# Kernel tuning notes

Measured on AMD Instinct MI355X. Metric: run time of the kernel, lower is better.

## Reference

```python
import jax, jax.numpy as jnp
import numpy as np
import math

B, T, C, H = 4, 2048, 1024, 16
D = C // H  # head dim


def setup_inputs() -> dict:
    key = jax.random.key(0)
    ks = jax.random.split(key, 8)
    s = 1.0 / math.sqrt(C)
    return {
        "q": jax.random.normal(ks[0], (B, T, C), jnp.float32),
        "k": jax.random.normal(ks[1], (B, T, C), jnp.float32),
        "v": jax.random.normal(ks[2], (B, T, C), jnp.float32),
        "Wq": jax.random.normal(ks[3], (C, C), jnp.float32) * s,
        "bq": jnp.zeros((C,), jnp.float32),
        "Wk": jax.random.normal(ks[4], (C, C), jnp.float32) * s,
        "bk": jnp.zeros((C,), jnp.float32),
        "Wv": jax.random.normal(ks[5], (C, C), jnp.float32) * s,
        "bv": jnp.zeros((C,), jnp.float32),
        "Wo": jax.random.normal(ks[6], (C, C), jnp.float32) * s,
        "bo": jnp.zeros((C,), jnp.float32),
    }


def reference(q, k, v, Wq, bq, Wk, bk, Wv, bv, Wo, bo):
    # Linear projections (torch Linear: x @ W.T + b; here W stored as [in,out])
    qh = (q @ Wq + bq).reshape(B, T, H, D).transpose(0, 2, 1, 3)  # [B,H,T,D]
    kh = (k @ Wk + bk).reshape(B, T, H, D).transpose(0, 2, 1, 3)
    vh = (v @ Wv + bv).reshape(B, T, H, D).transpose(0, 2, 1, 3)
    scores = jnp.einsum("bhqd,bhkd->bhqk", qh, kh) * (1.0 / math.sqrt(D))
    att = jax.nn.softmax(scores, axis=-1)
    y = jnp.einsum("bhqk,bhkd->bhqd", att, vh)  # [B,H,T,D]
    y = y.transpose(0, 2, 1, 3).reshape(B, T, C)
    return y @ Wo + bo
```

## Files before the change

kernel.cpp:

```cpp
#include <hip/hip_runtime.h>
#include <hip/hip_bf16.h>


#define B_ 4
#define T_ 2048
#define C_ 1024
#define H_ 16
#define D_ 64
#define M_ (B_*T_)

typedef __attribute__((ext_vector_type(4))) float f32x4;
typedef __attribute__((ext_vector_type(8))) short short8;

__device__ __forceinline__ unsigned short f2bf(float f) {
  unsigned u = __float_as_uint(f);
  u = (u + 0x7fffu + ((u >> 16) & 1u)) >> 16;
  return (unsigned short)u;
}

__device__ __forceinline__ unsigned cvtpk_bf16(float lo, float hi) {
  unsigned r;
  asm("v_cvt_pk_bf16_f32 %0, %1, %2" : "=v"(r) : "v"(lo), "v"(hi));
  return r;
}

__device__ __forceinline__ void gload_lds16(const void* g, void* l) {
  __builtin_amdgcn_global_load_lds(
      (__attribute__((address_space(1))) void*)(g),
      (__attribute__((address_space(3))) void*)(l), 16, 0, 0);
}

__global__ __launch_bounds__(256) void prep_all(const float* __restrict__ q,
                                                const float* __restrict__ k,
                                                const float* __restrict__ v,
                                                const float* __restrict__ W0,
                                                const float* __restrict__ W1,
                                                const float* __restrict__ W2,
                                                const float* __restrict__ W3,
                                                unsigned short* __restrict__ qb,
                                                unsigned short* __restrict__ kb,
                                                unsigned short* __restrict__ vb,
                                                unsigned short* __restrict__ T0,
                                                unsigned short* __restrict__ T1,
                                                unsigned short* __restrict__ T2,
                                                unsigned short* __restrict__ T3) {
  __shared__ float tile[64][65];
  const int id = blockIdx.x;
  if (id < 24576) {
    const int arr = id >> 13;
    const int blk = id & 8191;
    const float* s = (arr == 0) ? q : (arr == 1) ? k : v;
    unsigned short* d = (arr == 0) ? qb : (arr == 1) ? kb : vb;
    int i = blk * 256 + threadIdx.x;
    float4 x = ((const float4*)s)[i];
    ushort4 o = { f2bf(x.x), f2bf(x.y), f2bf(x.z), f2bf(x.w) };
    ((ushort4*)d)[i] = o;
  } else {
    const int tid = id - 24576;
    const int z = tid >> 8;
    const int tl = tid & 255;
    const float* W = (z == 0) ? W0 : (z == 1) ? W1 : (z == 2) ? W2 : W3;
    unsigned short* WT = (z == 0) ? T0 : (z == 1) ? T1 : (z == 2) ? T2 : T3;
    const int tr = (tl >> 4) * 64;
    const int tc = (tl & 15) * 64;
    const int t = threadIdx.x;
    const int cg = (t & 15) * 4;
    const int rw = t >> 4;
#pragma unroll
    for (int it = 0; it < 4; ++it) {
      int r = it * 16 + rw;
      float4 x = *(const float4*)(W + (size_t)(tr + r) * C_ + tc + cg);
      tile[r][cg] = x.x; tile[r][cg + 1] = x.y; tile[r][cg + 2] = x.z; tile[r][cg + 3] = x.w;
    }
    __syncthreads();
#pragma unroll
    for (int it = 0; it < 4; ++it) {
      int n = it * 16 + rw;
      ushort4 o = { f2bf(tile[cg][n]), f2bf(tile[cg + 1][n]),
                    f2bf(tile[cg + 2][n]), f2bf(tile[cg + 3][n]) };
      *(ushort4*)(WT + (size_t)(tc + n) * C_ + tr + cg) = o;
    }
  }
}

__device__ __forceinline__ void gemm_core(const unsigned short* __restrict__ A,
                                          const unsigned short* __restrict__ BT,
                                          int bm, int bn, int wid, int lane,
                                          unsigned short* As, unsigned short* Bs,
                                          f32x4 acc[4][4]) {
  const int wr = wid >> 1, wc = wid & 1;
  const int lr = lane & 15, lk = lane >> 4;
  for (int k0 = 0; k0 < C_; k0 += 64) {
    __syncthreads();
#pragma unroll
    for (int it = 0; it < 4; ++it) {
      int wo = it * 256 + wid * 64;
      int o = wo + lane;
      gload_lds16(A + (size_t)(bm * 128 + (o >> 3)) * C_ + k0 + (o & 7) * 8, As + wo * 8);
    }
#pragma unroll
    for (int it = 0; it < 4; ++it) {
      int wo = it * 256 + wid * 64;
      int o = wo + lane;
      gload_lds16(BT + (size_t)(bn * 128 + (o >> 3)) * C_ + k0 + (o & 7) * 8, Bs + wo * 8);
    }
    __syncthreads();

    short8 af[2][4], bf[2][4];
#pragma unroll
    for (int kc = 0; kc < 2; ++kc) {
#pragma unroll
      for (int mi = 0; mi < 4; ++mi)
        af[kc][mi] = *(const short8*)(As + (wr * 64 + mi * 16 + lr) * 64 + kc * 32 + lk * 8);
#pragma unroll
      for (int ni = 0; ni < 4; ++ni)
        bf[kc][ni] = *(const short8*)(Bs + (wc * 64 + ni * 16 + lr) * 64 + kc * 32 + lk * 8);
    }
#pragma unroll
    for (int kc = 0; kc < 2; ++kc)
#pragma unroll
      for (int mi = 0; mi < 4; ++mi)
#pragma unroll
        for (int ni = 0; ni < 4; ++ni)
          acc[mi][ni] = __builtin_amdgcn_mfma_f32_16x16x32_bf16(af[kc][mi], bf[kc][ni],
                                                                acc[mi][ni], 0, 0, 0);
  }
}

__global__ __launch_bounds__(256) void gemm_qkv(const unsigned short* __restrict__ qb,
                                                const unsigned short* __restrict__ kb,
                                                const unsigned short* __restrict__ vb,
                                                const unsigned short* __restrict__ wqt,
                                                const unsigned short* __restrict__ wkt,
                                                const unsigned short* __restrict__ wvt,
                                                const float* __restrict__ bq,
                                                const float* __restrict__ bk,
                                                const float* __restrict__ bv,
                                                unsigned short* __restrict__ Qh,
                                                unsigned short* __restrict__ Kh,
                                                unsigned short* __restrict__ VTh) {
  __shared__ unsigned short As[128 * 64];
  __shared__ unsigned short Bs[128 * 64];
  const int y = blockIdx.y;
  const unsigned short* A  = (y == 0) ? qb  : (y == 1) ? kb  : vb;
  const unsigned short* BT = (y == 0) ? wqt : (y == 1) ? wkt : wvt;
  const float* bias        = (y == 0) ? bq  : (y == 1) ? bk  : bv;
  unsigned short* O        = (y == 0) ? Qh  : (y == 1) ? Kh  : VTh;
  const bool vt = (y == 2);
  const int id = blockIdx.x;
  const int wk = (id & 7) * 64 + (id >> 3);
  const int bn = wk & 7;
  const int bm = wk >> 3;
  const int wid = threadIdx.x >> 6, lane = threadIdx.x & 63;
  const int wr = wid >> 1, wc = wid & 1;
  const int lr = lane & 15, lk = lane >> 4;
  f32x4 acc[4][4] = {};
  gemm_core(A, BT, bm, bn, wid, lane, As, Bs, acc);

  float bvv[4];
#pragma unroll
  for (int ni = 0; ni < 4; ++ni) bvv[ni] = bias[bn * 128 + wc * 64 + ni * 16 + lr];
#pragma unroll
  for (int mi = 0; mi < 4; ++mi)
#pragma unroll
    for (int ni = 0; ni < 4; ++ni) {
      int n = bn * 128 + wc * 64 + ni * 16 + lr;
      int h = n >> 6, d = n & 63;
#pragma unroll
      for (int j = 0; j < 4; ++j) {
        int m = bm * 128 + wr * 64 + mi * 16 + lk * 4 + j;
        int b = m >> 11, tt = m & (T_ - 1);
        size_t idx = vt ? ((size_t)(b * H_ + h) * D_ + d) * T_ + tt
                        : ((size_t)(b * H_ + h) * T_ + tt) * D_ + d;
        O[idx] = f2bf(acc[mi][ni][j] + bvv[ni]);
      }
    }
}

__global__ __launch_bounds__(256) void gemm_out(const unsigned short* __restrict__ A,
                                                const unsigned short* __restrict__ BT,
                                                const float* __restrict__ bias,
                                                float* __restrict__ O) {
  __shared__ unsigned short As[128 * 64];
  __shared__ unsigned short Bs[128 * 64];
  const int id = blockIdx.x;
  const int wk = (id & 7) * 64 + (id >> 3);
  const int bn = wk & 7;
  const int bm = wk >> 3;
  const int wid = threadIdx.x >> 6, lane = threadIdx.x & 63;
  const int wr = wid >> 1, wc = wid & 1;
  const int lr = lane & 15, lk = lane >> 4;
  f32x4 acc[4][4] = {};
  gemm_core(A, BT, bm, bn, wid, lane, As, Bs, acc);

  float bvv[4];
#pragma unroll
  for (int ni = 0; ni < 4; ++ni) bvv[ni] = bias[bn * 128 + wc * 64 + ni * 16 + lr];
#pragma unroll
  for (int mi = 0; mi < 4; ++mi)
#pragma unroll
    for (int ni = 0; ni < 4; ++ni) {
      int n = bn * 128 + wc * 64 + ni * 16 + lr;
#pragma unroll
      for (int j = 0; j < 4; ++j) {
        int m = bm * 128 + wr * 64 + mi * 16 + lk * 4 + j;
        O[(size_t)m * C_ + n] = acc[mi][ni][j] + bvv[ni];
      }
    }
}

__global__ __launch_bounds__(256) void attn_fwd(const unsigned short* __restrict__ Qg,
                                                const unsigned short* __restrict__ Kg,
                                                const unsigned short* __restrict__ Vg,
                                                unsigned short* __restrict__ Y) {
  __shared__ unsigned short Ks[2][64 * 64];
  __shared__ unsigned short Vs[2][64 * 64];
  __shared__ unsigned short Ps[64 * 64];
  const int id = blockIdx.x;
  const int wk = (id & 7) * 256 + (id >> 3);
  const int bh = wk >> 5;
  const int qt = wk & 31;
  const int b = bh >> 4, h = bh & 15;
  const int t = threadIdx.x;
  const int wid = t >> 6, lane = t & 63;
  const int lr = lane & 15, lk = lane >> 4;
  const size_t hoff = (size_t)bh * T_ * D_;
  const unsigned short* Qh = Qg + hoff + (size_t)qt * 64 * D_;
  const unsigned short* Kh = Kg + hoff;
  const unsigned short* Vh = Vg + hoff;
  const int NT = T_ / 64;

  auto stage = [&](int bfi, int kt) {
    const unsigned short* Ksrc = Kh + (size_t)kt * 64 * D_;
#pragma unroll
    for (int it = 0; it < 2; ++it) {
      int wo = it * 256 + wid * 64;
      int o = wo + lane;
      int r = o >> 3, c = (o & 7) ^ (r & 7);
      gload_lds16(Ksrc + (size_t)r * D_ + c * 8, Ks[bfi] + wo * 8);
      gload_lds16(Vh + (size_t)r * T_ + kt * 64 + c * 8, Vs[bfi] + wo * 8);
    }
  };

#pragma unroll
  for (int it = 0; it < 2; ++it) {
    int wo = it * 256 + wid * 64;
    int o = wo + lane;
    int r = o >> 3, c = (o & 7) ^ (r & 7);
    gload_lds16(Qh + (size_t)r * D_ + c * 8, Ps + wo * 8);
  }
  stage(0, 0);
  __syncthreads();
  short8 qf[2];
#pragma unroll
  for (int kc = 0; kc < 2; ++kc)
    qf[kc] = *(const short8*)(Ps + (wid * 16 + lr) * 64 + (((kc * 4 + lk) ^ (lr & 7)) * 8));
  asm volatile("s_waitcnt lgkmcnt(0)" ::: "memory");

  f32x4 yacc[4] = {};
  float mrow = -1e30f, lsum = 0.f;
  const float SCL = 0.125f;
  const float L2E = 1.44269504088896f;
  const float C1 = SCL * L2E;

  int cur = 0;
  for (int kt = 0; kt < NT; ++kt) {
    if (kt + 1 < NT) stage(cur ^ 1, kt + 1);

    f32x4 sacc[4] = {};
    __builtin_amdgcn_s_setprio(1);
#pragma unroll
    for (int kc = 0; kc < 2; ++kc)
#pragma unroll
      for (int nt = 0; nt < 4; ++nt) {
        short8 kf = *(const short8*)(Ks[cur] + (nt * 16 + lr) * 64 +
                                     (((kc * 4 + lk) ^ (lr & 7)) * 8));
        sacc[nt] = __builtin_amdgcn_mfma_f32_16x16x32_bf16(kf, qf[kc], sacc[nt], 0, 0, 0);
      }
    __builtin_amdgcn_s_setprio(0);

    float m0 = fmaxf(fmaxf(sacc[0][0], sacc[0][1]), fmaxf(sacc[0][2], sacc[0][3]));
#pragma unroll
    for (int nt = 1; nt < 4; ++nt)
      m0 = fmaxf(m0, fmaxf(fmaxf(sacc[nt][0], sacc[nt][1]),
                           fmaxf(sacc[nt][2], sacc[nt][3])));
    m0 = fmaxf(m0, __shfl_xor(m0, 16, 64));
    m0 = fmaxf(m0, __shfl_xor(m0, 32, 64));
    float mx = m0 * SCL;
    if (__any(mx - mrow > 8.0f)) {
      float mn = fmaxf(mrow, mx);
      float esc = exp2f((mrow - mn) * L2E);
      mrow = mn;
      lsum *= esc;
      float e0 = __shfl(esc, 4 * lk + 0, 16);
      float e1 = __shfl(esc, 4 * lk + 1, 16);
      float e2 = __shfl(esc, 4 * lk + 2, 16);
      float e3 = __shfl(esc, 4 * lk + 3, 16);
#pragma unroll
      for (int nt = 0; nt < 4; ++nt) {
        yacc[nt][0] *= e0; yacc[nt][1] *= e1;
        yacc[nt][2] *= e2; yacc[nt][3] *= e3;
      }
    }
    float ml2 = mrow * L2E;
    float rs = 0.f;
#pragma unroll
    for (int nt = 0; nt < 4; ++nt) {
      float p0 = exp2f(sacc[nt][0] * C1 - ml2);
      float p1 = exp2f(sacc[nt][1] * C1 - ml2);
      float p2 = exp2f(sacc[nt][2] * C1 - ml2);
      float p3 = exp2f(sacc[nt][3] * C1 - ml2);
      rs += (p0 + p1) + (p2 + p3);
      uint2 pv;
      pv.x = cvtpk_bf16(p0, p1);
      pv.y = cvtpk_bf16(p2, p3);
      *(uint2*)(Ps + (wid * 16 + lr) * 64 +
                (((2 * nt + (lk >> 1)) ^ (lr & 7)) * 8 + (lk & 1) * 4)) = pv;
    }
    rs += __shfl_xor(rs, 16, 64);
    rs += __shfl_xor(rs, 32, 64);
    lsum += rs;
    asm volatile("s_waitcnt lgkmcnt(0)" ::: "memory");

    __builtin_amdgcn_s_setprio(1);
#pragma unroll
    for (int kc = 0; kc < 2; ++kc) {
      short8 pa = *(const short8*)(Ps + (wid * 16 + lr) * 64 +
                                   (((kc * 4 + lk) ^ (lr & 7)) * 8));
#pragma unroll
      for (int nt = 0; nt < 4; ++nt) {
        short8 vf = *(const short8*)(Vs[cur] + (nt * 16 + lr) * 64 +
                                     (((kc * 4 + lk) ^ (lr & 7)) * 8));
        yacc[nt] = __builtin_amdgcn_mfma_f32_16x16x32_bf16(pa, vf, yacc[nt], 0, 0, 0);
      }
    }
    __builtin_amdgcn_s_setprio(0);

    __syncthreads();
    cur ^= 1;
  }

  float rinv = __builtin_amdgcn_rcpf(lsum);
  float r0 = __shfl(rinv, 4 * lk + 0, 16);
  float r1 = __shfl(rinv, 4 * lk + 1, 16);
  float r2 = __shfl(rinv, 4 * lk + 2, 16);
  float r3 = __shfl(rinv, 4 * lk + 3, 16);
#pragma unroll
  for (int nt = 0; nt < 4; ++nt) {
    int row = qt * 64 + wid * 16 + lk * 4;
    int col = h * D_ + nt * 16 + lr;
    size_t base = ((size_t)b * T_ + row) * C_ + col;
    Y[base]          = f2bf(yacc[nt][0] * r0);
    Y[base + C_]     = f2bf(yacc[nt][1] * r1);
    Y[base + 2 * C_] = f2bf(yacc[nt][2] * r2);
    Y[base + 3 * C_] = f2bf(yacc[nt][3] * r3);
  }
}

extern "C" void kernel_launch(void* const* d_in, const int* in_sizes, int n_in,
                              void* d_out, int out_size, void* d_ws, size_t ws_size,
                              hipStream_t stream) {
  const float* q  = (const float*)d_in[0];
  const float* k  = (const float*)d_in[1];
  const float* v  = (const float*)d_in[2];
  const float* Wq = (const float*)d_in[3];
  const float* bq = (const float*)d_in[4];
  const float* Wk = (const float*)d_in[5];
  const float* bk = (const float*)d_in[6];
  const float* Wv = (const float*)d_in[7];
  const float* bv = (const float*)d_in[8];
  const float* Wo = (const float*)d_in[9];
  const float* bo = (const float*)d_in[10];

  char* ws = (char*)d_ws;
  const size_t S1 = (size_t)M_ * C_ * 2;
  const size_t SW = (size_t)C_ * C_ * 2;
  unsigned short* qb  = (unsigned short*)(ws);
  unsigned short* kb  = (unsigned short*)(ws + S1);
  unsigned short* vb  = (unsigned short*)(ws + 2 * S1);
  unsigned short* wqt = (unsigned short*)(ws + 3 * S1);
  unsigned short* wkt = (unsigned short*)(ws + 3 * S1 + SW);
  unsigned short* wvt = (unsigned short*)(ws + 3 * S1 + 2 * SW);
  unsigned short* wot = (unsigned short*)(ws + 3 * S1 + 3 * SW);
  unsigned short* Qh  = (unsigned short*)(ws + 3 * S1 + 4 * SW);
  unsigned short* Kh  = (unsigned short*)(ws + 4 * S1 + 4 * SW);
  unsigned short* VTh = (unsigned short*)(ws + 5 * S1 + 4 * SW);
  unsigned short* Yw  = (unsigned short*)(ws + 6 * S1 + 4 * SW);

  prep_all<<<25600, 256, 0, stream>>>(q, k, v, Wq, Wk, Wv, Wo,
                                      qb, kb, vb, wqt, wkt, wvt, wot);

  const int ngemm = (C_ / 128) * (M_ / 128);
  gemm_qkv<<<dim3(ngemm, 3), 256, 0, stream>>>(qb, kb, vb, wqt, wkt, wvt,
                                               bq, bk, bv, Qh, Kh, VTh);

  attn_fwd<<<(T_ / 64) * B_ * H_, 256, 0, stream>>>(Qh, Kh, VTh, Yw);

  gemm_out<<<ngemm, 256, 0, stream>>>(Yw, wot, bo, (float*)d_out);
}
```

Before: 432.7 us.

## Split each key tile across two wave groups in attention with final merge

The attention block grows from 4 to 8 waves. Each pair of waves handles the same 16 query rows, but each wave processes a different 32-key half of every 64-key tile. Each wave keeps its own running max, sum and output accumulator, and the two partial results are combined through LDS in an online-softmax merge at the end. This roughly doubles the waves available to hide latency and halves the MFMA and softmax work per wave, at the cost of an extra LDS merge, a final barrier, and higher per-block thread and register demand.

```diff
diff --git a/kernel.cpp b/kernel.cpp
--- a/kernel.cpp
+++ b/kernel.cpp
@@ -209,7 +209,7 @@
     }
 }
 
-__global__ __launch_bounds__(256) void attn_fwd(const unsigned short* __restrict__ Qg,
+__global__ __launch_bounds__(512) void attn_fwd(const unsigned short* __restrict__ Qg,
                                                 const unsigned short* __restrict__ Kg,
                                                 const unsigned short* __restrict__ Vg,
                                                 unsigned short* __restrict__ Y) {
@@ -223,6 +223,7 @@
   const int b = bh >> 4, h = bh & 15;
   const int t = threadIdx.x;
   const int wid = t >> 6, lane = t & 63;
+  const int wq = wid & 3, kh = wid >> 2;
   const int lr = lane & 15, lk = lane >> 4;
   const size_t hoff = (size_t)bh * T_ * D_;
   const unsigned short* Qh = Qg + hoff + (size_t)qt * 64 * D_;
@@ -230,32 +231,23 @@
   const unsigned short* Vh = Vg + hoff;
   const int NT = T_ / 64;
 
+  const int o = wid * 64 + lane;
+  const int sr = o >> 3, sc = (o & 7) ^ ((o >> 3) & 7);
+  const int sbase = wid * 512;
+
   auto stage = [&](int bfi, int kt) {
-    const unsigned short* Ksrc = Kh + (size_t)kt * 64 * D_;
-#pragma unroll
-    for (int it = 0; it < 2; ++it) {
-      int wo = it * 256 + wid * 64;
-      int o = wo + lane;
-      int r = o >> 3, c = (o & 7) ^ (r & 7);
-      gload_lds16(Ksrc + (size_t)r * D_ + c * 8, Ks[bfi] + wo * 8);
-      gload_lds16(Vh + (size_t)r * T_ + kt * 64 + c * 8, Vs[bfi] + wo * 8);
-    }
+    gload_lds16(Kh + (size_t)kt * 64 * D_ + (size_t)sr * D_ + sc * 8, Ks[bfi] + sbase);
+    gload_lds16(Vh + (size_t)sr * T_ + kt * 64 + sc * 8, Vs[bfi] + sbase);
   };
 
-#pragma unroll
-  for (int it = 0; it < 2; ++it) {
-    int wo = it * 256 + wid * 64;
-    int o = wo + lane;
-    int r = o >> 3, c = (o & 7) ^ (r & 7);
-    gload_lds16(Qh + (size_t)r * D_ + c * 8, Ps + wo * 8);
-  }
+  gload_lds16(Qh + (size_t)sr * D_ + sc * 8, Ps + sbase);
   stage(0, 0);
   __syncthreads();
   short8 qf[2];
 #pragma unroll
   for (int kc = 0; kc < 2; ++kc)
-    qf[kc] = *(const short8*)(Ps + (wid * 16 + lr) * 64 + (((kc * 4 + lk) ^ (lr & 7)) * 8));
-  asm volatile("s_waitcnt lgkmcnt(0)" ::: "memory");
+    qf[kc] = *(const short8*)(Ps + (wq * 16 + lr) * 64 + (((kc * 4 + lk) ^ (lr & 7)) * 8));
+  __syncthreads();
 
   f32x4 yacc[4] = {};
   float mrow = -1e30f, lsum = 0.f;
@@ -267,23 +259,20 @@
   for (int kt = 0; kt < NT; ++kt) {
     if (kt + 1 < NT) stage(cur ^ 1, kt + 1);
 
-    f32x4 sacc[4] = {};
+    f32x4 sacc[2] = {};
     __builtin_amdgcn_s_setprio(1);
 #pragma unroll
     for (int kc = 0; kc < 2; ++kc)
 #pragma unroll
-      for (int nt = 0; nt < 4; ++nt) {
-        short8 kf = *(const short8*)(Ks[cur] + (nt * 16 + lr) * 64 +
+      for (int ntl = 0; ntl < 2; ++ntl) {
+        short8 kf = *(const short8*)(Ks[cur] + (kh * 32 + ntl * 16 + lr) * 64 +
                                      (((kc * 4 + lk) ^ (lr & 7)) * 8));
-        sacc[nt] = __builtin_amdgcn_mfma_f32_16x16x32_bf16(kf, qf[kc], sacc[nt], 0, 0, 0);
+        sacc[ntl] = __builtin_amdgcn_mfma_f32_16x16x32_bf16(kf, qf[kc], sacc[ntl], 0, 0, 0);
       }
     __builtin_amdgcn_s_setprio(0);
 
     float m0 = fmaxf(fmaxf(sacc[0][0], sacc[0][1]), fmaxf(sacc[0][2], sacc[0][3]));
-#pragma unroll
-    for (int nt = 1; nt < 4; ++nt)
-      m0 = fmaxf(m0, fmaxf(fmaxf(sacc[nt][0], sacc[nt][1]),
-                           fmaxf(sacc[nt][2], sacc[nt][3])));
+    m0 = fmaxf(m0, fmaxf(fmaxf(sacc[1][0], sacc[1][1]), fmaxf(sacc[1][2], sacc[1][3])));
     m0 = fmaxf(m0, __shfl_xor(m0, 16, 64));
     m0 = fmaxf(m0, __shfl_xor(m0, 32, 64));
     float mx = m0 * SCL;
@@ -305,17 +294,17 @@
     float ml2 = mrow * L2E;
     float rs = 0.f;
 #pragma unroll
-    for (int nt = 0; nt < 4; ++nt) {
-      float p0 = exp2f(sacc[nt][0] * C1 - ml2);
-      float p1 = exp2f(sacc[nt][1] * C1 - ml2);
-      float p2 = exp2f(sacc[nt][2] * C1 - ml2);
-      float p3 = exp2f(sacc[nt][3] * C1 - ml2);
+    for (int ntl = 0; ntl < 2; ++ntl) {
+      float p0 = exp2f(sacc[ntl][0] * C1 - ml2);
+      float p1 = exp2f(sacc[ntl][1] * C1 - ml2);
+      float p2 = exp2f(sacc[ntl][2] * C1 - ml2);
+      float p3 = exp2f(sacc[ntl][3] * C1 - ml2);
       rs += (p0 + p1) + (p2 + p3);
       uint2 pv;
       pv.x = cvtpk_bf16(p0, p1);
       pv.y = cvtpk_bf16(p2, p3);
-      *(uint2*)(Ps + (wid * 16 + lr) * 64 +
-                (((2 * nt + (lk >> 1)) ^ (lr & 7)) * 8 + (lk & 1) * 4)) = pv;
+      *(uint2*)(Ps + (wq * 16 + lr) * 64 +
+                (((kh * 4 + ntl * 2 + (lk >> 1)) ^ (lr & 7)) * 8 + (lk & 1) * 4)) = pv;
     }
     rs += __shfl_xor(rs, 16, 64);
     rs += __shfl_xor(rs, 32, 64);
@@ -323,16 +312,13 @@
     asm volatile("s_waitcnt lgkmcnt(0)" ::: "memory");
 
     __builtin_amdgcn_s_setprio(1);
-#pragma unroll
-    for (int kc = 0; kc < 2; ++kc) {
-      short8 pa = *(const short8*)(Ps + (wid * 16 + lr) * 64 +
-                                   (((kc * 4 + lk) ^ (lr & 7)) * 8));
-#pragma unroll
-      for (int nt = 0; nt < 4; ++nt) {
-        short8 vf = *(const short8*)(Vs[cur] + (nt * 16 + lr) * 64 +
-                                     (((kc * 4 + lk) ^ (lr & 7)) * 8));
-        yacc[nt] = __builtin_amdgcn_mfma_f32_16x16x32_bf16(pa, vf, yacc[nt], 0, 0, 0);
-      }
+    short8 pa = *(const short8*)(Ps + (wq * 16 + lr) * 64 +
+                                 (((kh * 4 + lk) ^ (lr & 7)) * 8));
+#pragma unroll
+    for (int nt = 0; nt < 4; ++nt) {
+      short8 vf = *(const short8*)(Vs[cur] + (nt * 16 + lr) * 64 +
+                                   (((kh * 4 + lk) ^ (lr & 7)) * 8));
+      yacc[nt] = __builtin_amdgcn_mfma_f32_16x16x32_bf16(pa, vf, yacc[nt], 0, 0, 0);
     }
     __builtin_amdgcn_s_setprio(0);
 
@@ -340,20 +326,37 @@
     cur ^= 1;
   }
 
-  float rinv = __builtin_amdgcn_rcpf(lsum);
-  float r0 = __shfl(rinv, 4 * lk + 0, 16);
-  float r1 = __shfl(rinv, 4 * lk + 1, 16);
-  float r2 = __shfl(rinv, 4 * lk + 2, 16);
-  float r3 = __shfl(rinv, 4 * lk + 3, 16);
-#pragma unroll
-  for (int nt = 0; nt < 4; ++nt) {
-    int row = qt * 64 + wid * 16 + lk * 4;
-    int col = h * D_ + nt * 16 + lr;
-    size_t base = ((size_t)b * T_ + row) * C_ + col;
-    Y[base]          = f2bf(yacc[nt][0] * r0);
-    Y[base + C_]     = f2bf(yacc[nt][1] * r1);
-    Y[base + 2 * C_] = f2bf(yacc[nt][2] * r2);
-    Y[base + 3 * C_] = f2bf(yacc[nt][3] * r3);
+  float* yb  = (float*)Ks;
+  float* sml = (float*)Vs;
+  if (kh == 1) {
+    if (lk == 0) { sml[wq * 16 + lr] = mrow; sml[64 + wq * 16 + lr] = lsum; }
+#pragma unroll
+    for (int nt = 0; nt < 4; ++nt)
+      *(f32x4*)&yb[(wq * 64 + lane) * 16 + nt * 4] = yacc[nt];
+  }
+  __syncthreads();
+  if (kh == 0) {
+    float m2 = sml[wq * 16 + lr], l2 = sml[64 + wq * 16 + lr];
+    float mf = fmaxf(mrow, m2);
+    float a  = exp2f((mrow - mf) * L2E);
+    float bb = exp2f((m2 - mf) * L2E);
+    float rv = __builtin_amdgcn_rcpf(a * lsum + bb * l2);
+    float ar = a * rv, br = bb * rv;
+    float a0 = __shfl(ar, 4 * lk + 0, 16), b0 = __shfl(br, 4 * lk + 0, 16);
+    float a1 = __shfl(ar, 4 * lk + 1, 16), b1 = __shfl(br, 4 * lk + 1, 16);
+    float a2 = __shfl(ar, 4 * lk + 2, 16), b2 = __shfl(br, 4 * lk + 2, 16);
+    float a3 = __shfl(ar, 4 * lk + 3, 16), b3 = __shfl(br, 4 * lk + 3, 16);
+#pragma unroll
+    for (int nt = 0; nt < 4; ++nt) {
+      f32x4 y2 = *(f32x4*)&yb[(wq * 64 + lane) * 16 + nt * 4];
+      int row = qt * 64 + wq * 16 + lk * 4;
+      int col = h * D_ + nt * 16 + lr;
+      size_t base = ((size_t)b * T_ + row) * C_ + col;
+      Y[base]          = f2bf(a0 * yacc[nt][0] + b0 * y2[0]);
+      Y[base + C_]     = f2bf(a1 * yacc[nt][1] + b1 * y2[1]);
+      Y[base + 2 * C_] = f2bf(a2 * yacc[nt][2] + b2 * y2[2]);
+      Y[base + 3 * C_] = f2bf(a3 * yacc[nt][3] + b3 * y2[3]);
+    }
   }
 }
 
@@ -394,7 +397,7 @@
   gemm_qkv<<<dim3(ngemm, 3), 256, 0, stream>>>(qb, kb, vb, wqt, wkt, wvt,
                                                bq, bk, bv, Qh, Kh, VTh);
 
-  attn_fwd<<<(T_ / 64) * B_ * H_, 256, 0, stream>>>(Qh, Kh, VTh, Yw);
+  attn_fwd<<<(T_ / 64) * B_ * H_, 512, 0, stream>>>(Qh, Kh, VTh, Yw);
 
   gemm_out<<<ngemm, 256, 0, stream>>>(Yw, wot, bo, (float*)d_out);
 }
```

Result: faster. 419.1 us (-3.1%).
